# Kernel optimization log

Hardware: AMD Instinct MI355X
Metric: run time of the kernel (lower is better)

Reference implementation:

```python
import jax, jax.numpy as jnp
import numpy as np
from jax import lax

# dims
B, T = 64, 1024
ANNOT, RNN, MEM, ATTN = 512, 1024, 512, 512
FILTERS, KSIZE = 32, 31
PAD = (KSIZE - 1) // 2  # 15, SAME padding


def setup_inputs() -> dict:
    key = jax.random.key(0)
    ks = jax.random.split(key, 20)
    s = 0.02
    return {
        "memory": jax.random.normal(ks[0], (B, MEM), jnp.float32),
        "context": jax.random.normal(ks[1], (B, ANNOT), jnp.float32),
        "rnn_state": jax.random.normal(ks[2], (B, RNN), jnp.float32),
        "annots": jax.random.normal(ks[3], (B, T, ANNOT), jnp.float32),
        "atten": jax.random.uniform(ks[4], (B, 2, T), jnp.float32),
        "mask": jnp.ones((B, T), jnp.int32),
        "t": 0,
        # GRUCell params (torch gate order: r, z, n)
        "W_ih": jax.random.normal(ks[5], (3 * RNN, ANNOT + MEM), jnp.float32) * s,
        "W_hh": jax.random.normal(ks[6], (3 * RNN, RNN), jnp.float32) * s,
        "b_ih": jnp.zeros((3 * RNN,), jnp.float32),
        "b_hh": jnp.zeros((3 * RNN,), jnp.float32),
        # location-sensitive attention params
        "conv_w": jax.random.normal(ks[7], (FILTERS, 2, KSIZE), jnp.float32) * s,
        "loc_w": jax.random.normal(ks[8], (ATTN, FILTERS), jnp.float32) * s,
        "loc_b": jnp.zeros((ATTN,), jnp.float32),
        "q_w": jax.random.normal(ks[9], (ATTN, RNN), jnp.float32) * s,
        "q_b": jnp.zeros((ATTN,), jnp.float32),
        "a_w": jax.random.normal(ks[10], (ATTN, ANNOT), jnp.float32) * s,
        "a_b": jnp.zeros((ATTN,), jnp.float32),
        "v_w": jax.random.normal(ks[11], (1, ATTN), jnp.float32) * s,
    }


def _gru_cell(x, h, W_ih, W_hh, b_ih, b_hh):
    gi = x @ W_ih.T + b_ih  # [B, 3H]
    gh = h @ W_hh.T + b_hh
    i_r, i_z, i_n = jnp.split(gi, 3, axis=-1)
    h_r, h_z, h_n = jnp.split(gh, 3, axis=-1)
    r = jax.nn.sigmoid(i_r + h_r)
    z = jax.nn.sigmoid(i_z + h_z)
    n = jnp.tanh(i_n + r * h_n)
    return (1.0 - z) * n + z * h


def reference(memory, context, rnn_state, annots, atten, mask, t,
              W_ih, W_hh, b_ih, b_hh, conv_w, loc_w, loc_b,
              q_w, q_b, a_w, a_b, v_w):
    # GRU step on [memory; prev_context]
    rnn_input = jnp.concatenate([memory, context], axis=-1)  # [B, MEM+ANNOT]
    rnn_output = _gru_cell(rnn_input, rnn_state, W_ih, W_hh, b_ih, b_hh)  # [B, RNN]

    # location features: SAME conv over [B, 2, T] -> [B, FILTERS, T]
    loc_conv = lax.conv_general_dilated(
        atten, conv_w, window_strides=(1,), padding=[(PAD, PAD)],
        dimension_numbers=("NCH", "OIH", "NCH"))
    processed_loc = jnp.einsum("bft,af->bta", loc_conv, loc_w) + loc_b  # [B,T,ATTN]

    processed_query = (rnn_output @ q_w.T + q_b)[:, None, :]            # [B,1,ATTN]
    processed_annots = jnp.einsum("btd,ad->bta", annots, a_w) + a_b     # [B,T,ATTN]

    energy = jnp.tanh(processed_query + processed_annots + processed_loc)
    alignment = jnp.einsum("bta,a->bt", energy, v_w[0])                 # [B,T]

    # mask fill with -inf where mask == 0
    alignment = jnp.where(mask == 0, -jnp.inf, alignment)

    # sigmoid-normalized attention weights
    sig = jax.nn.sigmoid(alignment)
    alignment = sig / jnp.sum(sig, axis=1, keepdims=True)               # [B,T]

    new_context = jnp.einsum("bt,btd->bd", alignment, annots)           # [B,ANNOT]
    return rnn_output, new_context, alignment
```

## Files before the change

kernel.cpp:

```cpp
#include <hip/hip_runtime.h>

typedef float f32x4 __attribute__((ext_vector_type(4)));
typedef short bf16x8 __attribute__((ext_vector_type(8)));

__device__ __forceinline__ unsigned int pk2(float a, float b) {
    unsigned int ua = __float_as_uint(a); ua += 0x7FFFu + ((ua >> 16) & 1u);
    unsigned int ub = __float_as_uint(b); ub += 0x7FFFu + ((ub >> 16) & 1u);
    return __builtin_amdgcn_perm(ub, ua, 0x07060302u);
}
__device__ __forceinline__ unsigned short bf16_rne(float a) {
    unsigned int ua = __float_as_uint(a);
    ua += 0x7FFFu + ((ua >> 16) & 1u);
    return (unsigned short)(ua >> 16);
}
__device__ __forceinline__ float tanh_fast(float x) {
    float e = __expf(x + x);
    return 1.f - 2.f / (e + 1.f);
}
__device__ __forceinline__ f32x4 mfma16(bf16x8 a, bf16x8 b, f32x4 c) {
    return __builtin_amdgcn_mfma_f32_16x16x32_bf16(a, b, c, 0, 0, 0);
}
__device__ __forceinline__ void ald16(const void* g, void* l) {
    __builtin_amdgcn_global_load_lds(
        (const __attribute__((address_space(1))) unsigned int*)g,
        (__attribute__((address_space(3))) unsigned int*)l, 16, 0, 0);
}

#define Q_WIH   786432
#define Q_WHH   1572864
#define Q_QW    1703936
#define Q_X2    1720320
#define Q_X1    1736704
#define Q_BAW   1802240
#define Q_BLW   1806336
#define Q_EB    1806464
#define NCVT    7057

__global__ __launch_bounds__(256) void k_prep(
    const float* __restrict__ Wih, const float* __restrict__ Whh,
    const float* __restrict__ qw, const float* __restrict__ rnn_state,
    const float* __restrict__ memory, const float* __restrict__ context,
    const float* __restrict__ aw, const float* __restrict__ lw,
    const float* __restrict__ ab, const float* __restrict__ lb,
    const float* __restrict__ atten, const float* __restrict__ convw,
    unsigned short* __restrict__ Wihb, unsigned short* __restrict__ Whhb,
    unsigned short* __restrict__ qwb, unsigned short* __restrict__ X2b,
    unsigned short* __restrict__ X1b, unsigned short* __restrict__ Bbig,
    float* __restrict__ ebias, unsigned short* __restrict__ Lconv)
{
    __shared__ float att_s[2 * 160];
    __shared__ float cw_s[1984];
    const int tid = threadIdx.x;
    if (blockIdx.x < NCVT) {
        int q = blockIdx.x * 256 + tid;
        if (q >= Q_EB) return;
        if (q < Q_WIH) {
            int i = q * 4;
            float4 v = *(const float4*)(Wih + i);
            uint2 u; u.x = pk2(v.x, v.y); u.y = pk2(v.z, v.w);
            *(uint2*)(Wihb + i) = u;
        } else if (q < Q_WHH) {
            int i = (q - Q_WIH) * 4;
            float4 v = *(const float4*)(Whh + i);
            uint2 u; u.x = pk2(v.x, v.y); u.y = pk2(v.z, v.w);
            *(uint2*)(Whhb + i) = u;
        } else if (q < Q_QW) {
            int i = (q - Q_WHH) * 4;
            float4 v = *(const float4*)(qw + i);
            uint2 u; u.x = pk2(v.x, v.y); u.y = pk2(v.z, v.w);
            *(uint2*)(qwb + i) = u;
        } else if (q < Q_X2) {
            int i = (q - Q_QW) * 4;
            float4 v = *(const float4*)(rnn_state + i);
            uint2 u; u.x = pk2(v.x, v.y); u.y = pk2(v.z, v.w);
            *(uint2*)(X2b + i) = u;
        } else if (q < Q_X1) {
            int i = (q - Q_X2) * 4;
            int b = i >> 10, c = i & 1023;
            const float* s = (c < 512) ? (memory + b * 512 + c) : (context + b * 512 + (c - 512));
            float4 v = *(const float4*)s;
            uint2 u; u.x = pk2(v.x, v.y); u.y = pk2(v.z, v.w);
            *(uint2*)(X1b + i) = u;
        } else if (q < Q_BAW) {
            int i = (q - Q_X1) * 4;
            int a = i >> 9, c = i & 511;
            float4 v = *(const float4*)(aw + a * 512 + c);
            uint2 u; u.x = pk2(v.x, v.y); u.y = pk2(v.z, v.w);
            *(uint2*)(Bbig + a * 544 + c) = u;
        } else if (q < Q_BLW) {
            int i = (q - Q_BAW) * 4;
            int a = i >> 5, c = i & 31;
            float4 v = *(const float4*)(lw + a * 32 + c);
            uint2 u; u.x = pk2(v.x, v.y); u.y = pk2(v.z, v.w);
            *(uint2*)(Bbig + a * 544 + 512 + c) = u;
        } else {
            int i = (q - Q_BLW) * 4;
            float4 va = *(const float4*)(ab + i);
            float4 vb = *(const float4*)(lb + i);
            float4 r; r.x = va.x + vb.x; r.y = va.y + vb.y; r.z = va.z + vb.z; r.w = va.w + vb.w;
            *(float4*)(ebias + i) = r;
        }
    } else {
        const int bid = blockIdx.x - NCVT;
        const int b = bid >> 3;
        const int tbase = (bid & 7) * 128;
        for (int i = tid; i < 320; i += 256) {
            int c = i / 160, j = i % 160;
            float v = 0.f;
            int pos = tbase - 15 + j;
            if (j < 158 && pos >= 0 && pos < 1024) v = atten[b * 2048 + c * 1024 + pos];
            att_s[c * 160 + j] = v;
        }
        for (int i = tid; i < 1984; i += 256) cw_s[i] = convw[i];
        __syncthreads();
        const int f = tid & 31, tq = tid >> 5;
        float acc[16];
#pragma unroll
        for (int i = 0; i < 16; ++i) acc[i] = 0.f;
        for (int c = 0; c < 2; ++c) {
            for (int k = 0; k < 31; ++k) {
                float w = cw_s[f * 62 + c * 31 + k];
                int base = c * 160 + tq * 16 + k;
#pragma unroll
                for (int ti = 0; ti < 16; ++ti) acc[ti] += w * att_s[base + ti];
            }
        }
#pragma unroll
        for (int ti = 0; ti < 16; ++ti) {
            int t = tbase + tq * 16 + ti;
            Lconv[(b * 1024 + t) * 32 + f] = bf16_rne(acc[ti]);
        }
    }
}

__global__ __launch_bounds__(256, 4) void k_gemm_ks(
    const unsigned short* __restrict__ A1, const unsigned short* __restrict__ A2,
    const unsigned short* __restrict__ B1, const unsigned short* __restrict__ B2,
    float* __restrict__ C, int N, int nTiles, int n_split, int K, int Klen)
{
    __shared__ __align__(16) unsigned short As[64 * 32];
    __shared__ __align__(16) unsigned short Bs[128 * 32];
    const int tid = threadIdx.x;
    const int nb = blockIdx.x % nTiles;
    const int ks = blockIdx.x / nTiles;
    const int nBase = nb * 128;
    const bool use2 = nBase >= n_split;
    const unsigned short* A = use2 ? A2 : A1;
    const unsigned short* B = use2 ? B2 : B1;
    const int brow0 = nBase - (use2 ? n_split : 0);
    const int lane = tid & 63, w = tid >> 6;
    const int c = lane & 15, qd = lane >> 4;
    const int lr = lane >> 2;
    const int swzl = ((lane & 3) ^ ((lr >> 1) & 3)) * 8;

    const f32x4 fz = {0.f, 0.f, 0.f, 0.f};
    f32x4 acc[4][2];
#pragma unroll
    for (int i = 0; i < 4; ++i) { acc[i][0] = fz; acc[i][1] = fz; }

    const int k0b = ks * Klen;
    const int nkc = Klen >> 5;
    for (int kc = 0; kc < nkc; ++kc) {
        const int k0 = k0b + kc * 32;
        ald16(A + (size_t)(w * 16 + lr) * K + k0 + swzl, &As[w * 512]);
        ald16(B + (size_t)(brow0 + w * 16 + lr) * K + k0 + swzl, &Bs[w * 512]);
        ald16(B + (size_t)(brow0 + 64 + w * 16 + lr) * K + k0 + swzl, &Bs[2048 + w * 512]);
        __syncthreads();
        const int rdoff = (qd ^ ((c >> 1) & 3)) * 8;
        bf16x8 af[4];
#pragma unroll
        for (int i = 0; i < 4; ++i) af[i] = *(const bf16x8*)&As[(i * 16 + c) * 32 + rdoff];
#pragma unroll
        for (int j = 0; j < 2; ++j) {
            bf16x8 bj = *(const bf16x8*)&Bs[(w * 32 + j * 16 + c) * 32 + rdoff];
#pragma unroll
            for (int i = 0; i < 4; ++i) acc[i][j] = mfma16(af[i], bj, acc[i][j]);
        }
        __syncthreads();
    }
    float* Cp = C + (size_t)ks * 64 * N;
#pragma unroll
    for (int i = 0; i < 4; ++i)
#pragma unroll
        for (int r = 0; r < 4; ++r) {
            int row = i * 16 + qd * 4 + r;
#pragma unroll
            for (int j = 0; j < 2; ++j) {
                int col = nBase + w * 32 + j * 16 + c;
                Cp[row * N + col] = acc[i][j][r];
            }
        }
}

__global__ __launch_bounds__(256) void k_gates(
    const float* __restrict__ Cg, const float* __restrict__ h0,
    const float* __restrict__ bih, const float* __restrict__ bhh,
    float* __restrict__ outv, unsigned short* __restrict__ X3b)
{
    int idx = blockIdx.x * 256 + threadIdx.x;
    int b = idx >> 10, h = idx & 1023;
    const float* g0 = Cg + b * 6144;
    const float* g1 = Cg + 393216 + b * 6144;
    float ir = g0[h] + g1[h] + bih[h];
    float iz = g0[h + 1024] + g1[h + 1024] + bih[h + 1024];
    float inn = g0[h + 2048] + g1[h + 2048] + bih[h + 2048];
    float hr = g0[h + 3072] + g1[h + 3072] + bhh[h];
    float hz = g0[h + 4096] + g1[h + 4096] + bhh[h + 1024];
    float hn = g0[h + 5120] + g1[h + 5120] + bhh[h + 2048];
    float r = 1.f / (1.f + __expf(-(ir + hr)));
    float z = 1.f / (1.f + __expf(-(iz + hz)));
    float n = tanh_fast(inn + r * hn);
    float o = (1.f - z) * n + z * h0[idx];
    outv[idx] = o;
    X3b[idx] = bf16_rne(o);
}

__global__ __launch_bounds__(256, 2) void k_attn(
    const float* __restrict__ annots, const unsigned short* __restrict__ Lconv,
    const unsigned short* __restrict__ Bbig, const float* __restrict__ pqP,
    const float* __restrict__ qb, const float* __restrict__ ebias,
    const float* __restrict__ vw, float* __restrict__ wsal)
{
    __shared__ __align__(16) unsigned short As[2][64 * 32];
    __shared__ __align__(16) unsigned short Bs[2][512 * 32];
    __shared__ float red[4][64];
    const int tid = threadIdx.x;
    const int btBase = blockIdx.x * 64;
    const int b = btBase >> 10;
    const int lane = tid & 63, w = tid >> 6;
    const int c = lane & 15, qd = lane >> 4;
    const int lr = lane >> 2;
    const int swzl = ((lane & 3) ^ ((lr >> 1) & 3)) * 8;
    const int arow = tid >> 2, alc = tid & 3;
    const int apofs = (alc ^ ((arow >> 1) & 3)) * 8;

    const f32x4 fz = {0.f, 0.f, 0.f, 0.f};
    f32x4 acc[4][8];
#pragma unroll
    for (int i = 0; i < 4; ++i)
#pragma unroll
        for (int j = 0; j < 8; ++j) acc[i][j] = fz;

    const float* aP = annots + (size_t)(btBase + arow) * 512 + alc * 8;
    const unsigned short* bP = Bbig + (size_t)(w * 16 + lr) * 544 + swzl;

#pragma unroll
    for (int s = 0; s < 8; ++s)
        ald16(bP + (size_t)s * 64 * 544, &Bs[0][s * 2048 + w * 512]);
    {
        float4 v0 = *(const float4*)(aP);
        float4 v1 = *(const float4*)(aP + 4);
        uint4 u;
        u.x = pk2(v0.x, v0.y); u.y = pk2(v0.z, v0.w);
        u.z = pk2(v1.x, v1.y); u.w = pk2(v1.z, v1.w);
        *(uint4*)&As[0][arow * 32 + apofs] = u;
    }
    __syncthreads();

    for (int kc = 0; kc < 17; ++kc) {
        const int cur = kc & 1, nxt = cur ^ 1;
        float4 v0n, v1n;
        if (kc < 16) {
            const int k1 = (kc + 1) * 32;
#pragma unroll
            for (int s = 0; s < 8; ++s)
                ald16(bP + (size_t)s * 64 * 544 + k1, &Bs[nxt][s * 2048 + w * 512]);
            if (kc < 15) {
                v0n = *(const float4*)(aP + k1);
                v1n = *(const float4*)(aP + k1 + 4);
            } else {
                ald16(Lconv + (size_t)(btBase + w * 16 + lr) * 32 + swzl, &As[nxt][w * 512]);
            }
        }
        const int rdoff = (qd ^ ((c >> 1) & 3)) * 8;
        bf16x8 af[4];
#pragma unroll
        for (int i = 0; i < 4; ++i) af[i] = *(const bf16x8*)&As[cur][(i * 16 + c) * 32 + rdoff];
        __builtin_amdgcn_s_setprio(1);
#pragma unroll
        for (int j = 0; j < 8; ++j) {
            bf16x8 bj = *(const bf16x8*)&Bs[cur][(w * 128 + j * 16 + c) * 32 + rdoff];
#pragma unroll
            for (int i = 0; i < 4; ++i) acc[i][j] = mfma16(af[i], bj, acc[i][j]);
        }
        __builtin_amdgcn_s_setprio(0);
        if (kc < 16) {
            if (kc < 15) {
                uint4 u;
                u.x = pk2(v0n.x, v0n.y); u.y = pk2(v0n.z, v0n.w);
                u.z = pk2(v1n.x, v1n.y); u.w = pk2(v1n.z, v1n.w);
                *(uint4*)&As[nxt][arow * 32 + apofs] = u;
            }
            __syncthreads();
        }
    }
    float pe[8], vv[8];
#pragma unroll
    for (int j = 0; j < 8; ++j) {
        int colg = w * 128 + j * 16 + c;
        pe[j] = pqP[b * 512 + colg] + pqP[32768 + b * 512 + colg] + qb[colg] + ebias[colg];
        vv[j] = vw[colg];
    }
#pragma unroll
    for (int i = 0; i < 4; ++i)
#pragma unroll
        for (int r = 0; r < 4; ++r) {
            float p = 0.f;
#pragma unroll
            for (int j = 0; j < 8; ++j)
                p += vv[j] * tanh_fast(acc[i][j][r] + pe[j]);
            p += __shfl_xor(p, 1);
            p += __shfl_xor(p, 2);
            p += __shfl_xor(p, 4);
            p += __shfl_xor(p, 8);
            if (c == 0) red[w][i * 16 + qd * 4 + r] = p;
        }
    __syncthreads();
    if (tid < 64)
        wsal[btBase + tid] = red[0][tid] + red[1][tid] + red[2][tid] + red[3][tid];
}

__global__ __launch_bounds__(256) void k_ctx(
    const float* __restrict__ annots, const float* __restrict__ wsal,
    const int* __restrict__ mask, float* __restrict__ out)
{
    __shared__ float al[1024];
    __shared__ float wsum[4];
    __shared__ float red[256];
    const int b = blockIdx.x >> 3;
    const int chunk = blockIdx.x & 7;
    const int tid = threadIdx.x;
    float lsum = 0.f;
#pragma unroll
    for (int p = 0; p < 4; ++p) {
        int t = p * 256 + tid;
        int bt = b * 1024 + t;
        float raw = wsal[bt];
        float s = (mask[bt] != 0) ? 1.f / (1.f + __expf(-raw)) : 0.f;
        al[t] = s;
        lsum += s;
    }
    for (int off = 32; off > 0; off >>= 1) lsum += __shfl_xor(lsum, off);
    if ((tid & 63) == 0) wsum[tid >> 6] = lsum;
    __syncthreads();
    const float tot = wsum[0] + wsum[1] + wsum[2] + wsum[3];
    const float inv = 1.f / tot;
    if (chunk == 0) {
#pragma unroll
        for (int p = 0; p < 4; ++p) {
            int t = p * 256 + tid;
            out[98304 + b * 1024 + t] = al[t] * inv;
        }
    }
    const int dq = tid & 63, tq = tid >> 6;
    const int d = chunk * 64 + dq;
    const float* ap = annots + (size_t)(b * 1024 + tq * 256) * 512 + d;
    float acc = 0.f;
#pragma unroll 4
    for (int t = 0; t < 256; ++t) acc += al[tq * 256 + t] * ap[(size_t)t * 512];
    red[tid] = acc;
    __syncthreads();
    if (tid < 64) {
        float s2 = red[tid] + red[64 + tid] + red[128 + tid] + red[192 + tid];
        out[65536 + b * 512 + chunk * 64 + tid] = s2 * inv;
    }
}

extern "C" void kernel_launch(void* const* d_in, const int* in_sizes, int n_in,
                              void* d_out, int out_size, void* d_ws, size_t ws_size,
                              hipStream_t stream) {
    const float* memory    = (const float*)d_in[0];
    const float* context   = (const float*)d_in[1];
    const float* rnn_state = (const float*)d_in[2];
    const float* annots    = (const float*)d_in[3];
    const float* atten     = (const float*)d_in[4];
    const int*   mask      = (const int*)d_in[5];
    const float* W_ih   = (const float*)d_in[7];
    const float* W_hh   = (const float*)d_in[8];
    const float* b_ih   = (const float*)d_in[9];
    const float* b_hh   = (const float*)d_in[10];
    const float* conv_w = (const float*)d_in[11];
    const float* loc_w  = (const float*)d_in[12];
    const float* loc_b  = (const float*)d_in[13];
    const float* q_w    = (const float*)d_in[14];
    const float* q_b    = (const float*)d_in[15];
    const float* a_w    = (const float*)d_in[16];
    const float* a_b    = (const float*)d_in[17];
    const float* v_w    = (const float*)d_in[18];
    float* out = (float*)d_out;

    char* w8 = (char*)d_ws;
    unsigned short* Lconv = (unsigned short*)(w8 + 0);
    unsigned short* Bbig  = (unsigned short*)(w8 + 4194304);
    unsigned short* Wihb  = (unsigned short*)(w8 + 4751360);
    unsigned short* Whhb  = (unsigned short*)(w8 + 11042816);
    unsigned short* qwb   = (unsigned short*)(w8 + 17334272);
    unsigned short* X1b   = (unsigned short*)(w8 + 18382848);
    unsigned short* X2b   = (unsigned short*)(w8 + 18513920);
    unsigned short* X3b   = (unsigned short*)(w8 + 18644992);
    float*          Cgru  = (float*)(w8 + 18776064);
    float*          pqP   = (float*)(w8 + 18776064);
    float*          wsal  = (float*)(w8 + 19038208);
    float*          ebias = (float*)(w8 + 21921792);

    k_prep<<<NCVT + 512, 256, 0, stream>>>(W_ih, W_hh, q_w, rnn_state, memory, context,
                                           a_w, loc_w, a_b, loc_b, atten, conv_w,
                                           Wihb, Whhb, qwb, X2b, X1b, Bbig, ebias, Lconv);
    k_gemm_ks<<<96, 256, 0, stream>>>(X1b, X2b, Wihb, Whhb, Cgru, 6144, 48, 3072, 1024, 512);
    k_gates<<<256, 256, 0, stream>>>(Cgru, rnn_state, b_ih, b_hh, out, X3b);
    k_gemm_ks<<<8, 256, 0, stream>>>(X3b, X3b, qwb, qwb, pqP, 512, 4, 0x40000000, 1024, 512);
    k_attn<<<1024, 256, 0, stream>>>(annots, Lconv, Bbig, pqP, q_b, ebias, v_w, wsal);
    k_ctx<<<512, 256, 0, stream>>>(annots, wsal, mask, out);
}
```

Before: 342.9 us.

## Load attention B operand directly to registers and widen split-K for query GEMM

In the attention kernel, the B-weight tiles now go from global memory straight into registers, double-buffered, instead of being staged in LDS. This removes the large LDS buffer, which could raise occupancy and cuts LDS traffic. Syncthreads is replaced by a manual lgkmcnt wait plus barrier, the Lconv tile is loaded through registers, and the k loop is fully unrolled. The query-projection GEMM now uses 32 blocks with a smaller K-split, so the attention kernel sums 8 partials. Each wave now issues redundant global loads of B, which relies on cache hits.

```diff
diff --git a/kernel.cpp b/kernel.cpp
--- a/kernel.cpp
+++ b/kernel.cpp
@@ -222,17 +222,15 @@
     const float* __restrict__ vw, float* __restrict__ wsal)
 {
     __shared__ __align__(16) unsigned short As[2][64 * 32];
-    __shared__ __align__(16) unsigned short Bs[2][512 * 32];
     __shared__ float red[4][64];
     const int tid = threadIdx.x;
     const int btBase = blockIdx.x * 64;
     const int b = btBase >> 10;
     const int lane = tid & 63, w = tid >> 6;
     const int c = lane & 15, qd = lane >> 4;
-    const int lr = lane >> 2;
-    const int swzl = ((lane & 3) ^ ((lr >> 1) & 3)) * 8;
     const int arow = tid >> 2, alc = tid & 3;
     const int apofs = (alc ^ ((arow >> 1) & 3)) * 8;
+    const int rdoff = (qd ^ ((c >> 1) & 3)) * 8;
 
     const f32x4 fz = {0.f, 0.f, 0.f, 0.f};
     f32x4 acc[4][8];
@@ -241,12 +239,12 @@
 #pragma unroll
         for (int j = 0; j < 8; ++j) acc[i][j] = fz;
 
+    const unsigned short* bBase = Bbig + (size_t)(w * 128 + c) * 544 + qd * 8;
     const float* aP = annots + (size_t)(btBase + arow) * 512 + alc * 8;
-    const unsigned short* bP = Bbig + (size_t)(w * 16 + lr) * 544 + swzl;
-
-#pragma unroll
-    for (int s = 0; s < 8; ++s)
-        ald16(bP + (size_t)s * 64 * 544, &Bs[0][s * 2048 + w * 512]);
+
+    bf16x8 bb[2][8];
+#pragma unroll
+    for (int j = 0; j < 8; ++j) bb[0][j] = *(const bf16x8*)(bBase + j * 8704);
     {
         float4 v0 = *(const float4*)(aP);
         float4 v1 = *(const float4*)(aP + 4);
@@ -255,34 +253,33 @@
         u.z = pk2(v1.x, v1.y); u.w = pk2(v1.z, v1.w);
         *(uint4*)&As[0][arow * 32 + apofs] = u;
     }
-    __syncthreads();
-
+    asm volatile("s_waitcnt lgkmcnt(0)" ::: "memory");
+    __builtin_amdgcn_s_barrier();
+    __builtin_amdgcn_sched_barrier(0);
+
+#pragma unroll
     for (int kc = 0; kc < 17; ++kc) {
         const int cur = kc & 1, nxt = cur ^ 1;
-        float4 v0n, v1n;
+        float4 v0n, v1n; uint4 lcv;
+        if (kc < 15) {
+            v0n = *(const float4*)(aP + (kc + 1) * 32);
+            v1n = *(const float4*)(aP + (kc + 1) * 32 + 4);
+        } else if (kc == 15) {
+            lcv = *(const uint4*)(Lconv + (size_t)(btBase + arow) * 32 + alc * 8);
+        }
         if (kc < 16) {
-            const int k1 = (kc + 1) * 32;
-#pragma unroll
-            for (int s = 0; s < 8; ++s)
-                ald16(bP + (size_t)s * 64 * 544 + k1, &Bs[nxt][s * 2048 + w * 512]);
-            if (kc < 15) {
-                v0n = *(const float4*)(aP + k1);
-                v1n = *(const float4*)(aP + k1 + 4);
-            } else {
-                ald16(Lconv + (size_t)(btBase + w * 16 + lr) * 32 + swzl, &As[nxt][w * 512]);
-            }
-        }
-        const int rdoff = (qd ^ ((c >> 1) & 3)) * 8;
+#pragma unroll
+            for (int j = 0; j < 8; ++j)
+                bb[nxt][j] = *(const bf16x8*)(bBase + j * 8704 + (kc + 1) * 32);
+        }
         bf16x8 af[4];
 #pragma unroll
         for (int i = 0; i < 4; ++i) af[i] = *(const bf16x8*)&As[cur][(i * 16 + c) * 32 + rdoff];
         __builtin_amdgcn_s_setprio(1);
 #pragma unroll
-        for (int j = 0; j < 8; ++j) {
-            bf16x8 bj = *(const bf16x8*)&Bs[cur][(w * 128 + j * 16 + c) * 32 + rdoff];
-#pragma unroll
-            for (int i = 0; i < 4; ++i) acc[i][j] = mfma16(af[i], bj, acc[i][j]);
-        }
+        for (int j = 0; j < 8; ++j)
+#pragma unroll
+            for (int i = 0; i < 4; ++i) acc[i][j] = mfma16(af[i], bb[cur][j], acc[i][j]);
         __builtin_amdgcn_s_setprio(0);
         if (kc < 16) {
             if (kc < 15) {
@@ -290,15 +287,22 @@
                 u.x = pk2(v0n.x, v0n.y); u.y = pk2(v0n.z, v0n.w);
                 u.z = pk2(v1n.x, v1n.y); u.w = pk2(v1n.z, v1n.w);
                 *(uint4*)&As[nxt][arow * 32 + apofs] = u;
+            } else {
+                *(uint4*)&As[nxt][arow * 32 + apofs] = lcv;
             }
-            __syncthreads();
+            asm volatile("s_waitcnt lgkmcnt(0)" ::: "memory");
+            __builtin_amdgcn_s_barrier();
+            __builtin_amdgcn_sched_barrier(0);
         }
     }
     float pe[8], vv[8];
 #pragma unroll
     for (int j = 0; j < 8; ++j) {
         int colg = w * 128 + j * 16 + c;
-        pe[j] = pqP[b * 512 + colg] + pqP[32768 + b * 512 + colg] + qb[colg] + ebias[colg];
+        float s = qb[colg] + ebias[colg];
+#pragma unroll
+        for (int p = 0; p < 8; ++p) s += pqP[p * 32768 + b * 512 + colg];
+        pe[j] = s;
         vv[j] = vw[colg];
     }
 #pragma unroll
@@ -400,7 +404,7 @@
     unsigned short* X3b   = (unsigned short*)(w8 + 18644992);
     float*          Cgru  = (float*)(w8 + 18776064);
     float*          pqP   = (float*)(w8 + 18776064);
-    float*          wsal  = (float*)(w8 + 19038208);
+    float*          wsal  = (float*)(w8 + 19824640);
     float*          ebias = (float*)(w8 + 21921792);
 
     k_prep<<<NCVT + 512, 256, 0, stream>>>(W_ih, W_hh, q_w, rnn_state, memory, context,
@@ -408,7 +412,7 @@
                                            Wihb, Whhb, qwb, X2b, X1b, Bbig, ebias, Lconv);
     k_gemm_ks<<<96, 256, 0, stream>>>(X1b, X2b, Wihb, Whhb, Cgru, 6144, 48, 3072, 1024, 512);
     k_gates<<<256, 256, 0, stream>>>(Cgru, rnn_state, b_ih, b_hh, out, X3b);
-    k_gemm_ks<<<8, 256, 0, stream>>>(X3b, X3b, qwb, qwb, pqP, 512, 4, 0x40000000, 1024, 512);
+    k_gemm_ks<<<32, 256, 0, stream>>>(X3b, X3b, qwb, qwb, pqP, 512, 4, 0x40000000, 1024, 128);
     k_attn<<<1024, 256, 0, stream>>>(annots, Lconv, Bbig, pqP, q_b, ebias, v_w, wsal);
     k_ctx<<<512, 256, 0, stream>>>(annots, wsal, mask, out);
 }
```

New measurement: 352.3 us. 1.03x slower.

## Enlarge attention tile to 256 rows with 16 waves sharing B tiles

Applied to the files above, without the earlier changes.

The attention-energy kernel now runs 1024-thread blocks on 256 rows. Sixteen waves are arranged 4x4 over rows and columns, so each staged weight tile is reused across four times more rows and total weight traffic from global memory drops. The query projection is split into 8 K-partials instead of 2, to give it more blocks, and the attention kernel sums all eight. The context reduction uses four independent accumulators to shorten the dependency chain. The cost is a heavier block: about 100KB of LDS and high register pressure at 1024 threads, which may limit occupancy or cause spills.

```diff
diff --git a/kernel.cpp b/kernel.cpp
--- a/kernel.cpp
+++ b/kernel.cpp
@@ -215,24 +215,26 @@
     X3b[idx] = bf16_rne(o);
 }
 
-__global__ __launch_bounds__(256, 2) void k_attn(
+__global__ __launch_bounds__(1024, 4) void k_attn(
     const float* __restrict__ annots, const unsigned short* __restrict__ Lconv,
     const unsigned short* __restrict__ Bbig, const float* __restrict__ pqP,
     const float* __restrict__ qb, const float* __restrict__ ebias,
     const float* __restrict__ vw, float* __restrict__ wsal)
 {
-    __shared__ __align__(16) unsigned short As[2][64 * 32];
+    __shared__ __align__(16) unsigned short As[2][256 * 32];
     __shared__ __align__(16) unsigned short Bs[2][512 * 32];
-    __shared__ float red[4][64];
+    __shared__ float red[16][64];
     const int tid = threadIdx.x;
-    const int btBase = blockIdx.x * 64;
+    const int btBase = blockIdx.x * 256;
     const int b = btBase >> 10;
     const int lane = tid & 63, w = tid >> 6;
+    const int wm = w & 3, wn = w >> 2;
     const int c = lane & 15, qd = lane >> 4;
     const int lr = lane >> 2;
     const int swzl = ((lane & 3) ^ ((lr >> 1) & 3)) * 8;
     const int arow = tid >> 2, alc = tid & 3;
     const int apofs = (alc ^ ((arow >> 1) & 3)) * 8;
+    const int rdoff = (qd ^ ((c >> 1) & 3)) * 8;
 
     const f32x4 fz = {0.f, 0.f, 0.f, 0.f};
     f32x4 acc[4][8];
@@ -242,11 +244,10 @@
         for (int j = 0; j < 8; ++j) acc[i][j] = fz;
 
     const float* aP = annots + (size_t)(btBase + arow) * 512 + alc * 8;
-    const unsigned short* bP = Bbig + (size_t)(w * 16 + lr) * 544 + swzl;
-
-#pragma unroll
-    for (int s = 0; s < 8; ++s)
-        ald16(bP + (size_t)s * 64 * 544, &Bs[0][s * 2048 + w * 512]);
+    const unsigned short* bP = Bbig + (size_t)(w * 32 + lr) * 544 + swzl;
+
+    ald16(bP, &Bs[0][(w * 32) * 32]);
+    ald16(bP + 16 * 544, &Bs[0][(w * 32 + 16) * 32]);
     {
         float4 v0 = *(const float4*)(aP);
         float4 v1 = *(const float4*)(aP + 4);
@@ -259,27 +260,26 @@
 
     for (int kc = 0; kc < 17; ++kc) {
         const int cur = kc & 1, nxt = cur ^ 1;
-        float4 v0n, v1n;
         if (kc < 16) {
             const int k1 = (kc + 1) * 32;
-#pragma unroll
-            for (int s = 0; s < 8; ++s)
-                ald16(bP + (size_t)s * 64 * 544 + k1, &Bs[nxt][s * 2048 + w * 512]);
-            if (kc < 15) {
-                v0n = *(const float4*)(aP + k1);
-                v1n = *(const float4*)(aP + k1 + 4);
-            } else {
-                ald16(Lconv + (size_t)(btBase + w * 16 + lr) * 32 + swzl, &As[nxt][w * 512]);
-            }
-        }
-        const int rdoff = (qd ^ ((c >> 1) & 3)) * 8;
+            ald16(bP + k1, &Bs[nxt][(w * 32) * 32]);
+            ald16(bP + 16 * 544 + k1, &Bs[nxt][(w * 32 + 16) * 32]);
+        }
+        float4 v0n, v1n;
+        if (kc < 15) {
+            v0n = *(const float4*)(aP + (kc + 1) * 32);
+            v1n = *(const float4*)(aP + (kc + 1) * 32 + 4);
+        } else if (kc == 15) {
+            ald16(Lconv + (size_t)(btBase + w * 16 + lr) * 32 + swzl, &As[nxt][w * 512]);
+        }
         bf16x8 af[4];
 #pragma unroll
-        for (int i = 0; i < 4; ++i) af[i] = *(const bf16x8*)&As[cur][(i * 16 + c) * 32 + rdoff];
+        for (int i = 0; i < 4; ++i)
+            af[i] = *(const bf16x8*)&As[cur][(wm * 64 + i * 16 + c) * 32 + rdoff];
         __builtin_amdgcn_s_setprio(1);
 #pragma unroll
         for (int j = 0; j < 8; ++j) {
-            bf16x8 bj = *(const bf16x8*)&Bs[cur][(w * 128 + j * 16 + c) * 32 + rdoff];
+            bf16x8 bj = *(const bf16x8*)&Bs[cur][(wn * 128 + j * 16 + c) * 32 + rdoff];
 #pragma unroll
             for (int i = 0; i < 4; ++i) acc[i][j] = mfma16(af[i], bj, acc[i][j]);
         }
@@ -297,8 +297,11 @@
     float pe[8], vv[8];
 #pragma unroll
     for (int j = 0; j < 8; ++j) {
-        int colg = w * 128 + j * 16 + c;
-        pe[j] = pqP[b * 512 + colg] + pqP[32768 + b * 512 + colg] + qb[colg] + ebias[colg];
+        int colg = wn * 128 + j * 16 + c;
+        float s = qb[colg] + ebias[colg];
+#pragma unroll
+        for (int p = 0; p < 8; ++p) s += pqP[p * 32768 + b * 512 + colg];
+        pe[j] = s;
         vv[j] = vw[colg];
     }
 #pragma unroll
@@ -316,8 +319,11 @@
             if (c == 0) red[w][i * 16 + qd * 4 + r] = p;
         }
     __syncthreads();
-    if (tid < 64)
-        wsal[btBase + tid] = red[0][tid] + red[1][tid] + red[2][tid] + red[3][tid];
+    if (tid < 256) {
+        const int band = tid >> 6, idx = tid & 63;
+        wsal[btBase + band * 64 + idx] =
+            red[band][idx] + red[band + 4][idx] + red[band + 8][idx] + red[band + 12][idx];
+    }
 }
 
 __global__ __launch_bounds__(256) void k_ctx(
@@ -355,14 +361,20 @@
     const int dq = tid & 63, tq = tid >> 6;
     const int d = chunk * 64 + dq;
     const float* ap = annots + (size_t)(b * 1024 + tq * 256) * 512 + d;
-    float acc = 0.f;
+    const float* alp = al + tq * 256;
+    float s0 = 0.f, s1 = 0.f, s2 = 0.f, s3 = 0.f;
 #pragma unroll 4
-    for (int t = 0; t < 256; ++t) acc += al[tq * 256 + t] * ap[(size_t)t * 512];
-    red[tid] = acc;
+    for (int t = 0; t < 256; t += 4) {
+        s0 += alp[t]     * ap[(size_t)(t)     * 512];
+        s1 += alp[t + 1] * ap[(size_t)(t + 1) * 512];
+        s2 += alp[t + 2] * ap[(size_t)(t + 2) * 512];
+        s3 += alp[t + 3] * ap[(size_t)(t + 3) * 512];
+    }
+    red[tid] = (s0 + s1) + (s2 + s3);
     __syncthreads();
     if (tid < 64) {
-        float s2 = red[tid] + red[64 + tid] + red[128 + tid] + red[192 + tid];
-        out[65536 + b * 512 + chunk * 64 + tid] = s2 * inv;
+        float s2r = red[tid] + red[64 + tid] + red[128 + tid] + red[192 + tid];
+        out[65536 + b * 512 + chunk * 64 + tid] = s2r * inv;
     }
 }
 
@@ -400,7 +412,7 @@
     unsigned short* X3b   = (unsigned short*)(w8 + 18644992);
     float*          Cgru  = (float*)(w8 + 18776064);
     float*          pqP   = (float*)(w8 + 18776064);
-    float*          wsal  = (float*)(w8 + 19038208);
+    float*          wsal  = (float*)(w8 + 19824640);
     float*          ebias = (float*)(w8 + 21921792);
 
     k_prep<<<NCVT + 512, 256, 0, stream>>>(W_ih, W_hh, q_w, rnn_state, memory, context,
@@ -408,7 +420,7 @@
                                            Wihb, Whhb, qwb, X2b, X1b, Bbig, ebias, Lconv);
     k_gemm_ks<<<96, 256, 0, stream>>>(X1b, X2b, Wihb, Whhb, Cgru, 6144, 48, 3072, 1024, 512);
     k_gates<<<256, 256, 0, stream>>>(Cgru, rnn_state, b_ih, b_hh, out, X3b);
-    k_gemm_ks<<<8, 256, 0, stream>>>(X3b, X3b, qwb, qwb, pqP, 512, 4, 0x40000000, 1024, 512);
-    k_attn<<<1024, 256, 0, stream>>>(annots, Lconv, Bbig, pqP, q_b, ebias, v_w, wsal);
+    k_gemm_ks<<<32, 256, 0, stream>>>(X3b, X3b, qwb, qwb, pqP, 512, 4, 0x40000000, 1024, 128);
+    k_attn<<<256, 1024, 0, stream>>>(annots, Lconv, Bbig, pqP, q_b, ebias, v_w, wsal);
     k_ctx<<<512, 256, 0, stream>>>(annots, wsal, mask, out);
 }
```

Result: slower. 645.6 us (+88.3%).
